# Performance work log

Measured on AMD Instinct MI355X. Metric: run time of the kernel, lower is better.

Reference implementation:

```python
import jax, jax.numpy as jnp
import numpy as np

NUM_CLASSES = 20
NUM_ANCHORS = 3
BBOX_ATTRS = 5 + NUM_CLASSES
IMG_H = IMG_W = 416
IN_H = IN_W = 52
CONF_THRES = 0.5
NMS_THRES = 0.4
TOP_K = 2048


def setup_inputs() -> dict:
    key = jax.random.key(0)
    k1, _ = jax.random.split(key)
    inp = jax.random.normal(k1, (16, NUM_ANCHORS * BBOX_ATTRS, IN_H, IN_W), dtype=jnp.float32)
    anchors = jnp.array([[116.0, 90.0], [156.0, 198.0], [373.0, 326.0]], dtype=jnp.float32)
    return {"input": inp, "anchors": anchors}


def decode(inp, anchors):
    """YOLOv3 head decode (YOLOv3Loss.forward with targets=None).
    inp: [B, A*(5+C), H, W] -> output: [B, A*H*W, 5+C] with (cx, cy, w, h, conf, cls...)."""
    bs = inp.shape[0]
    stride_h = IMG_H / IN_H
    stride_w = IMG_W / IN_W
    scaled_anchors = anchors / jnp.array([stride_w, stride_h], dtype=inp.dtype)  # [A, 2]
    # [B, A, H, W, 5+C]
    pred = inp.reshape(bs, NUM_ANCHORS, BBOX_ATTRS, IN_H, IN_W).transpose(0, 1, 3, 4, 2)
    x = jax.nn.sigmoid(pred[..., 0])
    y = jax.nn.sigmoid(pred[..., 1])
    w = pred[..., 2]
    h = pred[..., 3]
    conf = jax.nn.sigmoid(pred[..., 4])
    pred_cls = jax.nn.sigmoid(pred[..., 5:])
    grid_x = jnp.arange(IN_W, dtype=inp.dtype)[None, None, None, :]
    grid_y = jnp.arange(IN_H, dtype=inp.dtype)[None, None, :, None]
    anchor_w = scaled_anchors[:, 0][None, :, None, None]
    anchor_h = scaled_anchors[:, 1][None, :, None, None]
    bx = (x + grid_x) * stride_w
    by = (y + grid_y) * stride_h
    bw = jnp.exp(w) * anchor_w * stride_w
    bh = jnp.exp(h) * anchor_h * stride_h
    boxes = jnp.stack([bx, by, bw, bh], axis=-1).reshape(bs, -1, 4)
    output = jnp.concatenate(
        [boxes, conf.reshape(bs, -1, 1), pred_cls.reshape(bs, -1, NUM_CLASSES)], axis=-1
    )
    return output


def _nms_one(corners, conf, cls_pred):
    """Greedy class-aware NMS over TOP_K conf-sorted candidates.
    corners: [K,4] x1y1x2y2, conf: [K] desc-sorted, cls_pred: [K] int32.
    Returns keep mask [K] bool."""
    x1, y1, x2, y2 = corners[:, 0], corners[:, 1], corners[:, 2], corners[:, 3]
    area = (x2 - x1 + 1.0) * (y2 - y1 + 1.0)
    ix1 = jnp.maximum(x1[:, None], x1[None, :])
    iy1 = jnp.maximum(y1[:, None], y1[None, :])
    ix2 = jnp.minimum(x2[:, None], x2[None, :])
    iy2 = jnp.minimum(y2[:, None], y2[None, :])
    inter = jnp.clip(ix2 - ix1 + 1.0, 0.0) * jnp.clip(iy2 - iy1 + 1.0, 0.0)
    iou = inter / (area[:, None] + area[None, :] - inter + 1e-16)
    # suppress j if kept i (earlier, higher conf, same class) overlaps >= thres
    cond = (iou >= NMS_THRES) & (cls_pred[:, None] == cls_pred[None, :])
    valid = conf >= CONF_THRES
    K = conf.shape[0]
    idx = jnp.arange(K)

    def body(i, carry):
        keep, supp = carry
        ki = valid[i] & (~supp[i])
        keep = keep.at[i].set(ki)
        supp = supp | (cond[i] & (idx > i) & ki)
        return keep, supp

    keep, _ = jax.lax.fori_loop(0, K, body, (jnp.zeros(K, bool), jnp.zeros(K, bool)))
    return keep


def reference(input, anchors):
    output = decode(input, anchors)  # [B, N, 5+C]
    conf = output[..., 4]
    # top-K candidates by objectness (desc order == conf sort in original NMS)
    top_conf, top_idx = jax.lax.top_k(conf, TOP_K)  # [B, K]
    boxes = output[..., :4]
    cx, cy, w, h = boxes[..., 0], boxes[..., 1], boxes[..., 2], boxes[..., 3]
    corners = jnp.stack([cx - w / 2, cy - h / 2, cx + w / 2, cy + h / 2], axis=-1)
    corners_s = jnp.take_along_axis(corners, top_idx[..., None], axis=1)  # [B, K, 4]
    cls_pred = jnp.argmax(output[..., 5:], axis=-1).astype(jnp.int32)  # [B, N]
    cls_s = jnp.take_along_axis(cls_pred, top_idx, axis=1)  # [B, K]
    keep = jax.vmap(_nms_one)(corners_s, top_conf, cls_s)  # [B, K] bool
    return output, top_idx, keep
```

## Files before the change

kernel.cpp:

```cpp
#include <hip/hip_runtime.h>

#pragma clang fp contract(off)

#define B 16
#define A 3
#define HGT 52
#define WID 52
#define HW 2704
#define NCAND 8112
#define CATTR 25
#define TOPK 2048
#define NWORD 64
#define CH 256
#define NCHUNK (TOPK / CH)
#define GPC (CH / 32)
#define CHP 260
#define EPT 8

typedef unsigned int uint32;
typedef unsigned long long u64;

__global__ __launch_bounds__(256) void decode_kernel(const float* __restrict__ inp,
                                                     const float* __restrict__ anchors,
                                                     float* __restrict__ out,
                                                     float* __restrict__ cws) {
    __shared__ float sm[256 * CATTR];
    int tid = threadIdx.x;
    int t = blockIdx.x * 256 + tid;
    int b  = t / NCAND;
    int n  = t - b * NCAND;
    int a  = n / HW;
    int hw = n - a * HW;
    int gy = hw / WID;
    int gx = hw - gy * WID;
    const float* ip = inp + ((size_t)(b * (A * CATTR) + a * CATTR)) * HW + hw;
    float* sp = sm + tid * CATTR;

    float p0 = ip[0 * HW], p1 = ip[1 * HW], p2 = ip[2 * HW], p3 = ip[3 * HW], p4 = ip[4 * HW];
    float sx = 1.0f / (1.0f + expf(-p0));
    float sy = 1.0f / (1.0f + expf(-p1));
    float bx = (sx + (float)gx) * 8.0f;
    float by = (sy + (float)gy) * 8.0f;
    float bw = expf(p2) * anchors[a * 2 + 0];
    float bh = expf(p3) * anchors[a * 2 + 1];
    float cf = 1.0f / (1.0f + expf(-p4));
    sp[0] = bx; sp[1] = by; sp[2] = bw; sp[3] = bh; sp[4] = cf;
    cws[t] = cf;
#pragma unroll
    for (int c = 0; c < 20; ++c) {
        float v = ip[(5 + c) * HW];
        sp[5 + c] = 1.0f / (1.0f + expf(-v));
    }
    __syncthreads();
    const float4* sm4 = (const float4*)sm;
    float4* o4 = (float4*)(out + (size_t)blockIdx.x * 256 * CATTR);
#pragma unroll
    for (int k = 0; k < 6; ++k) o4[k * 256 + tid] = sm4[k * 256 + tid];
    if (tid < 64) o4[1536 + tid] = sm4[1536 + tid];
}

__device__ __forceinline__ void cexd(u64& a, u64& b, bool up) {
    if ((a > b) == up) { u64 tmp = a; a = b; b = tmp; }
}

__device__ __forceinline__ u64 sel(u64 k, u64 o, bool kmin) {
    return kmin ? (k < o ? k : o) : (k > o ? k : o);
}

__device__ __forceinline__ void bitonic_merge_2048(u64 key[EPT], u64* mb, int t) {
    for (unsigned j = 1024; j >= 8; j >>= 1) {
        unsigned m = j >> 3;
        bool kmin = ((t & m) == 0);
        if (m >= 64) {
            __syncthreads();
#pragma unroll
            for (int e = 0; e < EPT; ++e) mb[e * 256 + t] = key[e];
            __syncthreads();
            int pt = t ^ (int)m;
#pragma unroll
            for (int e = 0; e < EPT; ++e) key[e] = sel(key[e], mb[e * 256 + pt], kmin);
        } else {
#pragma unroll
            for (int e = 0; e < EPT; ++e) {
                u64 o = __shfl_xor(key[e], (int)m);
                key[e] = sel(key[e], o, kmin);
            }
        }
    }
    cexd(key[0], key[4], true); cexd(key[1], key[5], true);
    cexd(key[2], key[6], true); cexd(key[3], key[7], true);
    cexd(key[0], key[2], true); cexd(key[1], key[3], true);
    cexd(key[4], key[6], true); cexd(key[5], key[7], true);
    cexd(key[0], key[1], true); cexd(key[2], key[3], true);
    cexd(key[4], key[5], true); cexd(key[6], key[7], true);
}

__global__ __launch_bounds__(256) void sort1_kernel(const float* __restrict__ conf,
                                                    u64* __restrict__ runs) {
    __shared__ u64 mb[2048];
    int blk = blockIdx.x;
    int b = blk >> 2, c = blk & 3;
    int t = threadIdx.x;
    int base = t * EPT;
    int gbase = c * 2048 + base;
    const float* cp = conf + b * NCAND;

    u64 key[EPT];
    if (gbase + EPT <= NCAND) {
        const float4* cp4 = (const float4*)(cp + gbase);
        float4 c0 = cp4[0], c1 = cp4[1];
        float cf[EPT] = {c0.x, c0.y, c0.z, c0.w, c1.x, c1.y, c1.z, c1.w};
#pragma unroll
        for (int e = 0; e < EPT; ++e) {
            unsigned bits = __float_as_uint(cf[e]) | 0x80000000u;
            key[e] = ((u64)(~bits) << 32) | (unsigned)(gbase + e);
        }
    } else {
#pragma unroll
        for (int e = 0; e < EPT; ++e) {
            int idx = gbase + e;
            if (idx < NCAND) {
                unsigned bits = __float_as_uint(cp[idx]) | 0x80000000u;
                key[e] = ((u64)(~bits) << 32) | (unsigned)idx;
            } else key[e] = ~0ull;
        }
    }

    cexd(key[0], key[1], true); cexd(key[2], key[3], false);
    cexd(key[4], key[5], true); cexd(key[6], key[7], false);

    cexd(key[0], key[2], true);  cexd(key[1], key[3], true);
    cexd(key[4], key[6], false); cexd(key[5], key[7], false);
    cexd(key[0], key[1], true);  cexd(key[2], key[3], true);
    cexd(key[4], key[5], false); cexd(key[6], key[7], false);

    bool up8 = ((t & 1) == 0);
    cexd(key[0], key[4], up8); cexd(key[1], key[5], up8);
    cexd(key[2], key[6], up8); cexd(key[3], key[7], up8);
    cexd(key[0], key[2], up8); cexd(key[1], key[3], up8);
    cexd(key[4], key[6], up8); cexd(key[5], key[7], up8);
    cexd(key[0], key[1], up8); cexd(key[2], key[3], up8);
    cexd(key[4], key[5], up8); cexd(key[6], key[7], up8);

    for (unsigned k = 16; k <= 2048; k <<= 1) {
        bool up = (((unsigned)base & k) == 0);
        for (unsigned j = k >> 1; j >= 8; j >>= 1) {
            unsigned m = j >> 3;
            bool kmin = (up == ((t & m) == 0));
            if (m >= 64) {
                __syncthreads();
#pragma unroll
                for (int e = 0; e < EPT; ++e) mb[e * 256 + t] = key[e];
                __syncthreads();
                int pt = t ^ (int)m;
#pragma unroll
                for (int e = 0; e < EPT; ++e) key[e] = sel(key[e], mb[e * 256 + pt], kmin);
            } else {
#pragma unroll
                for (int e = 0; e < EPT; ++e) {
                    u64 o = __shfl_xor(key[e], (int)m);
                    key[e] = sel(key[e], o, kmin);
                }
            }
        }
        cexd(key[0], key[4], up); cexd(key[1], key[5], up);
        cexd(key[2], key[6], up); cexd(key[3], key[7], up);
        cexd(key[0], key[2], up); cexd(key[1], key[3], up);
        cexd(key[4], key[6], up); cexd(key[5], key[7], up);
        cexd(key[0], key[1], up); cexd(key[2], key[3], up);
        cexd(key[4], key[5], up); cexd(key[6], key[7], up);
    }

    u64* R = runs + ((size_t)b * 4 + c) * 2048;
#pragma unroll
    for (int e = 0; e < EPT; ++e) R[base + e] = key[e];
}

__global__ __launch_bounds__(256) void sort23_kernel(const u64* __restrict__ runs,
                                                     const float* __restrict__ out,
                                                     float* __restrict__ topf,
                                                     float* __restrict__ gx1,
                                                     float* __restrict__ gy1,
                                                     float* __restrict__ gx2,
                                                     float* __restrict__ gy2,
                                                     float* __restrict__ gar,
                                                     uint32* __restrict__ gcv,
                                                     uint32* __restrict__ vwords) {
    __shared__ u64 mb[2048];
    __shared__ uint32 vb[256];
    int b = blockIdx.x;
    int t = threadIdx.x;
    int base = t * EPT;
    const u64* R0 = runs + (size_t)b * 4 * 2048;

    u64 ka[EPT], kb[EPT];
#pragma unroll
    for (int e = 0; e < EPT; ++e) {
        u64 a = R0[base + e];
        u64 o = R0[2048 + 2047 - (base + e)];
        ka[e] = a < o ? a : o;
    }
    bitonic_merge_2048(ka, mb, t);
#pragma unroll
    for (int e = 0; e < EPT; ++e) {
        u64 a = R0[2 * 2048 + base + e];
        u64 o = R0[3 * 2048 + 2047 - (base + e)];
        kb[e] = a < o ? a : o;
    }
    bitonic_merge_2048(kb, mb, t);
    __syncthreads();
#pragma unroll
    for (int e = 0; e < EPT; ++e) mb[base + e] = kb[e];
    __syncthreads();
#pragma unroll
    for (int e = 0; e < EPT; ++e) {
        u64 o = mb[2047 - (base + e)];
        ka[e] = ka[e] < o ? ka[e] : o;
    }
    bitonic_merge_2048(ka, mb, t);

    const float* ob = out + (size_t)b * NCAND * CATTR;
    uint32 vbits = 0;
#pragma unroll
    for (int e = 0; e < EPT; ++e) {
        uint32 idx = (uint32)(ka[e] & 0xFFFFFFFFu);
        int tg = b * TOPK + base + e;
        topf[tg] = (float)idx;
        const float* p = ob + (size_t)idx * CATTR;
        float cx = p[0], cy = p[1], w = p[2], h = p[3], cf = p[4];
        float hw_ = w * 0.5f, hh_ = h * 0.5f;
        float x1 = cx - hw_, y1 = cy - hh_, x2 = cx + hw_, y2 = cy + hh_;
        gx1[tg] = x1; gy1[tg] = y1; gx2[tg] = x2; gy2[tg] = y2;
        gar[tg] = ((x2 - x1) + 1.0f) * ((y2 - y1) + 1.0f);
        float best = p[5]; int bc = 0;
#pragma unroll
        for (int c = 1; c < 20; ++c) {
            float v = p[5 + c];
            if (v > best) { best = v; bc = c; }
        }
        gcv[tg] = (uint32)bc;
        vbits |= (cf >= 0.5f ? 1u : 0u) << e;
    }
    vb[t] = vbits;
    __syncthreads();
    if (t < 64) {
        uint32 w4 = vb[t * 4] | (vb[t * 4 + 1] << 8) | (vb[t * 4 + 2] << 16) | (vb[t * 4 + 3] << 24);
        vwords[b * 64 + t] = w4;
    }
}

#define KMID (13421772.5 / 33554432.0)
__global__ __launch_bounds__(1024) void build_kernel(const float* __restrict__ gx1,
                                                     const float* __restrict__ gy1,
                                                     const float* __restrict__ gx2,
                                                     const float* __restrict__ gy2,
                                                     const float* __restrict__ gar,
                                                     const uint32* __restrict__ gcv,
                                                     uint32* __restrict__ rowmask) {
    __shared__ float  x1s[TOPK], y1s[TOPK], x2s[TOPK], y2s[TOPK];
    __shared__ uint32 clss[TOPK];
    int bt   = blockIdx.y;
    int pr   = blockIdx.x;
    int tid  = threadIdx.x;
    int lane = tid & 63;
    int wv   = tid >> 6;
    int base = bt * TOPK;
    uint32* rmT = rowmask + (size_t)base * NWORD;

    for (int j = tid; j < TOPK; j += 1024) {
        int g = base + j;
        x1s[j] = gx1[g]; y1s[j] = gy1[g]; x2s[j] = gx2[g]; y2s[j] = gy2[g];
        clss[j] = gcv[g] & 0xffu;
    }
    __syncthreads();

    int r  = (wv >> 3) ? (31 - pr) : pr;
    int i0 = r * 64 + (wv & 7) * 8;

    float rx1[8], ry1[8], rx2[8], ry2[8], rar[8];
    uint32 rcl[8];
#pragma unroll
    for (int k = 0; k < 8; ++k) {
        rx1[k] = x1s[i0 + k]; ry1[k] = y1s[i0 + k];
        rx2[k] = x2s[i0 + k]; ry2[k] = y2s[i0 + k];
        rar[k] = ((rx2[k] - rx1[k]) + 1.0f) * ((ry2[k] - ry1[k]) + 1.0f);
        rcl[k] = clss[i0 + k];
    }

    int j0 = r * 64 + lane;
    float cx1 = x1s[j0], cy1 = y1s[j0], cx2 = x2s[j0], cy2 = y2s[j0];
    uint32 cc = clss[j0];

    for (int cg = r; cg < 32; ++cg) {
        float nx1 = 0.f, ny1 = 0.f, nx2 = 0.f, ny2 = 0.f; uint32 nc = 0;
        if (cg + 1 < 32) {
            int nj = (cg + 1) * 64 + lane;
            nx1 = x1s[nj]; ny1 = y1s[nj]; nx2 = x2s[nj]; ny2 = y2s[nj];
            nc = clss[nj];
        }
        float car = ((cx2 - cx1) + 1.0f) * ((cy2 - cy1) + 1.0f);
        u64 bal[8];
#pragma unroll
        for (int k = 0; k < 8; ++k) {
            float ix1 = fmaxf(rx1[k], cx1);
            float iy1 = fmaxf(ry1[k], cy1);
            float ix2 = fminf(rx2[k], cx2);
            float iy2 = fminf(ry2[k], cy2);
            float iw = fmaxf((ix2 - ix1) + 1.0f, 0.0f);
            float ih = fmaxf((iy2 - iy1) + 1.0f, 0.0f);
            float inter = iw * ih;
            float denom = ((rar[k] + car) - inter) + 1e-16f;
            bool cond = ((double)inter > KMID * (double)denom) && (cc == rcl[k]);
            bal[k] = __ballot(cond);
        }
        u64 v = bal[0];
#pragma unroll
        for (int k = 1; k < 8; ++k) if ((lane & 7) == k) v = bal[k];
        uint32 w32 = (lane & 8) ? (uint32)(v >> 32) : (uint32)v;
        int gi = i0 + (lane & 7);
        int wd = 2 * cg + ((lane >> 3) & 1);
        if (wd == (gi >> 5)) w32 &= ~((2u << (gi & 31)) - 1u);
        if (lane < 16) rmT[(size_t)wd * TOPK + gi] = w32;
        cx1 = nx1; cy1 = ny1; cx2 = nx2; cy2 = ny2; cc = nc;
    }
}

__device__ __forceinline__ void copy_chunk_dma(const uint32* __restrict__ rmT,
                                               uint32* dstL, int c, int wvm1, int lane) {
    int wmin = 8 * c;
    for (int w = wmin + wvm1; w < 64; w += 15) {
        const uint32* gp = rmT + (size_t)w * TOPK + c * CH + lane * 4;
        uint32* lp = dstL + w * CHP;
        __builtin_amdgcn_global_load_lds((const __attribute__((address_space(1))) void*)gp,
                                         (__attribute__((address_space(3))) void*)lp,
                                         16, 0, 0);
    }
}

__global__ __launch_bounds__(1024) void scan_kernel(const uint32* __restrict__ rowmask,
                                                    const uint32* __restrict__ vwords,
                                                    float* __restrict__ keepf) {
    __shared__ uint32 buf[2][64 * CHP];
    int bt  = blockIdx.x;
    int tid = threadIdx.x;
    int wv  = tid >> 6;
    int l   = tid & 63;
    const uint32* rmT = rowmask + (size_t)bt * TOPK * NWORD;

    uint32 supp = 0, keepw = 0;
    if (wv == 0) supp = ~vwords[bt * 64 + l];

    if (wv > 0) copy_chunk_dma(rmT, buf[0], 0, wv - 1, l);
    __syncthreads();

    for (int c = 0; c < NCHUNK; ++c) {
        if (wv > 0) {
            if (c + 1 < NCHUNK) copy_chunk_dma(rmT, buf[(c + 1) & 1], c + 1, wv - 1, l);
        } else {
            const uint32* bp = buf[c & 1];
            uint4 sq[8];
            {
                int g0 = c * GPC;
                const uint4* sp = (const uint4*)(bp + g0 * CHP);
#pragma unroll
                for (int q = 0; q < 8; ++q) sq[q] = sp[q];
            }
            for (int gl = 0; gl < GPC; ++gl) {
                int g = c * GPC + gl;
                uint4 rwq[8];
                const uint4* rp = (const uint4*)(bp + l * CHP + gl * 32);
#pragma unroll
                for (int q = 0; q < 8; ++q) rwq[q] = rp[q];
                uint32 cur = __builtin_amdgcn_readlane(supp, g);
#pragma unroll
                for (int q = 0; q < 8; ++q) {
                    uint32 s0 = sq[q].x, s1 = sq[q].y, s2 = sq[q].z, s3 = sq[q].w;
                    int k = q * 4;
                    cur |= s0 & ((((cur >> (k + 0)) & 1u)) - 1u);
                    cur |= s1 & ((((cur >> (k + 1)) & 1u)) - 1u);
                    cur |= s2 & ((((cur >> (k + 2)) & 1u)) - 1u);
                    cur |= s3 & ((((cur >> (k + 3)) & 1u)) - 1u);
                }
                uint32 keep = ~cur;
                if (l == g) keepw = keep;
                if (gl + 1 < GPC) {
                    const uint4* sp = (const uint4*)(bp + (g + 1) * CHP + (gl + 1) * 32);
#pragma unroll
                    for (int q = 0; q < 8; ++q) sq[q] = sp[q];
                }
                uint32 upd = 0;
#pragma unroll
                for (int q = 0; q < 8; ++q) {
                    int k = q * 4;
                    upd |= rwq[q].x & (uint32)(((int)(keep << (31 - (k + 0)))) >> 31);
                    upd |= rwq[q].y & (uint32)(((int)(keep << (31 - (k + 1)))) >> 31);
                    upd |= rwq[q].z & (uint32)(((int)(keep << (31 - (k + 2)))) >> 31);
                    upd |= rwq[q].w & (uint32)(((int)(keep << (31 - (k + 3)))) >> 31);
                }
                supp |= upd;
            }
        }
        __syncthreads();
    }

    if (wv == 0) {
#pragma unroll
        for (int k = 0; k < 32; ++k)
            keepf[bt * TOPK + l * 32 + k] = (float)((keepw >> k) & 1u);
    }
}

extern "C" void kernel_launch(void* const* d_in, const int* in_sizes, int n_in,
                              void* d_out, int out_size, void* d_ws, size_t ws_size,
                              hipStream_t stream) {
    const float* inp     = (const float*)d_in[0];
    const float* anchors = (const float*)d_in[1];
    float* out   = (float*)d_out;
    float* topf  = out  + (size_t)B * NCAND * CATTR;
    float* keepf = topf + (size_t)B * TOPK;

    float*  cws = (float*)d_ws;
    float*  gx1 = cws + B * NCAND;
    float*  gy1 = gx1 + B * TOPK;
    float*  gx2 = gy1 + B * TOPK;
    float*  gy2 = gx2 + B * TOPK;
    float*  gar = gy2 + B * TOPK;
    uint32* gcv = (uint32*)(gar + B * TOPK);
    uint32* rowmask = gcv + B * TOPK;
    uint32* vwords  = rowmask + (size_t)B * TOPK * NWORD;
    u64* runs = (u64*)rowmask;

    decode_kernel<<<(B * NCAND) / 256, 256, 0, stream>>>(inp, anchors, out, cws);
    sort1_kernel<<<B * 4, 256, 0, stream>>>(cws, runs);
    sort23_kernel<<<B, 256, 0, stream>>>(runs, out, topf, gx1, gy1, gx2, gy2, gar, gcv, vwords);
    build_kernel<<<dim3(16, B), 1024, 0, stream>>>(gx1, gy1, gx2, gy2, gar, gcv, rowmask);
    scan_kernel<<<B, 1024, 0, stream>>>(rowmask, vwords, keepf);
}
```

Baseline: 184.3 us.

## Precompute NMS box records in decode and gather them in a wide kernel

```diff
diff --git a/kernel.cpp b/kernel.cpp
--- a/kernel.cpp
+++ b/kernel.cpp
@@ -23,7 +23,8 @@
 __global__ __launch_bounds__(256) void decode_kernel(const float* __restrict__ inp,
                                                      const float* __restrict__ anchors,
                                                      float* __restrict__ out,
-                                                     float* __restrict__ cws) {
+                                                     float* __restrict__ cws,
+                                                     float* __restrict__ pk) {
     __shared__ float sm[256 * CATTR];
     int tid = threadIdx.x;
     int t = blockIdx.x * 256 + tid;
@@ -46,11 +47,23 @@
     float cf = 1.0f / (1.0f + expf(-p4));
     sp[0] = bx; sp[1] = by; sp[2] = bw; sp[3] = bh; sp[4] = cf;
     cws[t] = cf;
+
+    float best = -1.0f; int bc = 0;
 #pragma unroll
     for (int c = 0; c < 20; ++c) {
         float v = ip[(5 + c) * HW];
-        sp[5 + c] = 1.0f / (1.0f + expf(-v));
-    }
+        float s = 1.0f / (1.0f + expf(-v));
+        sp[5 + c] = s;
+        if (s > best) { best = s; bc = c; }
+    }
+
+    float hw_ = bw * 0.5f, hh_ = bh * 0.5f;
+    float x1 = bx - hw_, y1 = by - hh_, x2 = bx + hw_, y2 = by + hh_;
+    float area = ((x2 - x1) + 1.0f) * ((y2 - y1) + 1.0f);
+    float4* pk4 = (float4*)(pk + (size_t)t * 8);
+    pk4[0] = make_float4(x1, y1, x2, y2);
+    pk4[1] = make_float4(area, (float)bc, (cf >= 0.5f) ? 1.0f : 0.0f, 0.0f);
+
     __syncthreads();
     const float4* sm4 = (const float4*)sm;
     float4* o4 = (float4*)(out + (size_t)blockIdx.x * 256 * CATTR);
@@ -177,17 +190,8 @@
 }
 
 __global__ __launch_bounds__(256) void sort23_kernel(const u64* __restrict__ runs,
-                                                     const float* __restrict__ out,
-                                                     float* __restrict__ topf,
-                                                     float* __restrict__ gx1,
-                                                     float* __restrict__ gy1,
-                                                     float* __restrict__ gx2,
-                                                     float* __restrict__ gy2,
-                                                     float* __restrict__ gar,
-                                                     uint32* __restrict__ gcv,
-                                                     uint32* __restrict__ vwords) {
+                                                     float* __restrict__ topf) {
     __shared__ u64 mb[2048];
-    __shared__ uint32 vb[256];
     int b = blockIdx.x;
     int t = threadIdx.x;
     int base = t * EPT;
@@ -219,33 +223,33 @@
     }
     bitonic_merge_2048(ka, mb, t);
 
-    const float* ob = out + (size_t)b * NCAND * CATTR;
-    uint32 vbits = 0;
-#pragma unroll
-    for (int e = 0; e < EPT; ++e) {
-        uint32 idx = (uint32)(ka[e] & 0xFFFFFFFFu);
-        int tg = b * TOPK + base + e;
-        topf[tg] = (float)idx;
-        const float* p = ob + (size_t)idx * CATTR;
-        float cx = p[0], cy = p[1], w = p[2], h = p[3], cf = p[4];
-        float hw_ = w * 0.5f, hh_ = h * 0.5f;
-        float x1 = cx - hw_, y1 = cy - hh_, x2 = cx + hw_, y2 = cy + hh_;
-        gx1[tg] = x1; gy1[tg] = y1; gx2[tg] = x2; gy2[tg] = y2;
-        gar[tg] = ((x2 - x1) + 1.0f) * ((y2 - y1) + 1.0f);
-        float best = p[5]; int bc = 0;
-#pragma unroll
-        for (int c = 1; c < 20; ++c) {
-            float v = p[5 + c];
-            if (v > best) { best = v; bc = c; }
-        }
-        gcv[tg] = (uint32)bc;
-        vbits |= (cf >= 0.5f ? 1u : 0u) << e;
-    }
-    vb[t] = vbits;
-    __syncthreads();
-    if (t < 64) {
-        uint32 w4 = vb[t * 4] | (vb[t * 4 + 1] << 8) | (vb[t * 4 + 2] << 16) | (vb[t * 4 + 3] << 24);
-        vwords[b * 64 + t] = w4;
+#pragma unroll
+    for (int e = 0; e < EPT; ++e)
+        topf[(size_t)b * TOPK + base + e] = (float)(unsigned)(ka[e] & 0xFFFFFFFFu);
+}
+
+__global__ __launch_bounds__(256) void geo_kernel(const float* __restrict__ pk,
+                                                  const float* __restrict__ topf,
+                                                  float* __restrict__ gx1,
+                                                  float* __restrict__ gy1,
+                                                  float* __restrict__ gx2,
+                                                  float* __restrict__ gy2,
+                                                  float* __restrict__ gar,
+                                                  uint32* __restrict__ gcv,
+                                                  uint32* __restrict__ vwords) {
+    int t = blockIdx.x * 256 + threadIdx.x;
+    int b = t >> 11;
+    int idx = (int)topf[t];
+    const float4* p4 = (const float4*)(pk + ((size_t)b * NCAND + idx) * 8);
+    float4 g0 = p4[0], g1 = p4[1];
+    gx1[t] = g0.x; gy1[t] = g0.y; gx2[t] = g0.z; gy2[t] = g0.w;
+    gar[t] = g1.x;
+    gcv[t] = (uint32)g1.y;
+    bool valid = (g1.z != 0.0f);
+    unsigned long long bal = __ballot(valid);
+    if ((t & 63) == 0) {
+        vwords[(t >> 5) + 0] = (uint32)bal;
+        vwords[(t >> 5) + 1] = (uint32)(bal >> 32);
     }
 }
 
@@ -420,7 +424,8 @@
     float* keepf = topf + (size_t)B * TOPK;
 
     float*  cws = (float*)d_ws;
-    float*  gx1 = cws + B * NCAND;
+    float*  pk  = cws + B * NCAND;
+    float*  gx1 = pk  + (size_t)B * NCAND * 8;
     float*  gy1 = gx1 + B * TOPK;
     float*  gx2 = gy1 + B * TOPK;
     float*  gy2 = gx2 + B * TOPK;
@@ -430,9 +435,10 @@
     uint32* vwords  = rowmask + (size_t)B * TOPK * NWORD;
     u64* runs = (u64*)rowmask;
 
-    decode_kernel<<<(B * NCAND) / 256, 256, 0, stream>>>(inp, anchors, out, cws);
+    decode_kernel<<<(B * NCAND) / 256, 256, 0, stream>>>(inp, anchors, out, cws, pk);
     sort1_kernel<<<B * 4, 256, 0, stream>>>(cws, runs);
-    sort23_kernel<<<B, 256, 0, stream>>>(runs, out, topf, gx1, gy1, gx2, gy2, gar, gcv, vwords);
+    sort23_kernel<<<B, 256, 0, stream>>>(runs, topf);
+    geo_kernel<<<(B * TOPK) / 256, 256, 0, stream>>>(pk, topf, gx1, gy1, gx2, gy2, gar, gcv, vwords);
     build_kernel<<<dim3(16, B), 1024, 0, stream>>>(gx1, gy1, gx2, gy2, gar, gcv, rowmask);
     scan_kernel<<<B, 1024, 0, stream>>>(rowmask, vwords, keepf);
 }
```

After: 175.3 us. -4.9%, faster.
